# Optimization experiments

Hardware: AMD Instinct MI355X
Metric: run time of the kernel (lower is better)

## Reference

```python
import jax, jax.numpy as jnp
import numpy as np

K = 1024       # num_embeddings
D = 64         # embedding_dim
DECAY = 0.99
COMMIT = 0.25
EPS = 1e-05


def setup_inputs() -> dict:
    key = jax.random.key(0)
    k1, k2, k3 = jax.random.split(key, 3)
    x = jax.random.normal(k1, (16, 64, 64, 64), jnp.float32)  # NCHW, C == D
    embedding_weight = jax.random.normal(k2, (K, D), jnp.float32)
    ema_weight = jax.random.normal(k3, (K, D), jnp.float32)
    ema_cluster_size = jnp.zeros((K,), jnp.float32)
    return {"x": x, "embedding_weight": embedding_weight,
            "ema_cluster_size": ema_cluster_size, "ema_weight": ema_weight}


def reference(x, embedding_weight, ema_cluster_size, ema_weight):
    # NCHW -> NHWC, flatten tokens
    xp = jnp.transpose(x, (0, 2, 3, 1))            # [B,H,W,D]
    flat = xp.reshape(-1, D)                        # [N,D]
    dists = ((flat ** 2).sum(1, keepdims=True)
             + (embedding_weight ** 2).sum(1)
             - 2.0 * flat @ embedding_weight.T)     # [N,K]
    idx = jnp.argmin(dists, axis=1)                 # [N]
    encodings = jax.nn.one_hot(idx, K, dtype=flat.dtype)  # [N,K]
    quantized = jnp.take(embedding_weight, idx, axis=0).reshape(xp.shape)
    # training-mode EMA updates (scatter-add instead of dense one-hot matmuls)
    counts = jnp.zeros((K,), flat.dtype).at[idx].add(1.0)
    new_cs = ema_cluster_size * DECAY + (1.0 - DECAY) * counts
    n = new_cs.sum()
    new_cs = (new_cs + EPS) / (n + K * EPS) * n     # Laplace smoothing
    dw = jnp.zeros((K, D), flat.dtype).at[idx].add(flat)
    new_ema_weight = ema_weight * DECAY + (1.0 - DECAY) * dw
    new_embedding = new_ema_weight / new_cs[:, None]
    # commitment loss and straight-through estimator
    e_latent_loss = jnp.mean((jax.lax.stop_gradient(quantized) - xp) ** 2)
    loss = COMMIT * e_latent_loss
    q_st = xp + jax.lax.stop_gradient(quantized - xp)
    return (loss, jnp.transpose(q_st, (0, 3, 1, 2)), encodings,
            new_embedding, new_cs, new_ema_weight)
```

## Files before the change

kernel.cpp:

```cpp
#include <hip/hip_runtime.h>

#define HW 4096
#define DECAYF 0.99f
#define ONEMF 0.01f
#define EPSF 1e-5f
#define BIAS 192.0f

typedef __bf16 bf16x8 __attribute__((ext_vector_type(8)));
typedef float f32x4 __attribute__((ext_vector_type(4)));
typedef unsigned short ushort8 __attribute__((ext_vector_type(8)));

#define WS_DW     0
#define WS_COUNTS 1048576
#define WS_NCHALF 1064960
#define WS_SSE    1065984
#define WS_IDX    1066000
#define WS_EHI    1131536
#define WS_ELO    1164304

__device__ __forceinline__ float wave_reduce_add(float v) {
#pragma unroll
    for (int o = 32; o > 0; o >>= 1) v += __shfl_xor(v, o, 64);
    return v;
}

__device__ __forceinline__ unsigned short bf_rne(float f) {
    unsigned int u = __float_as_uint(f);
    unsigned int r = u + 0x7fffu + ((u >> 16) & 1u);
    return (unsigned short)(r >> 16);
}

__device__ __forceinline__ unsigned med3u(unsigned a, unsigned b, unsigned c) {
    unsigned mn = a < b ? a : b;
    unsigned mx = a > b ? a : b;
    unsigned t = mx < c ? mx : c;
    return mn > t ? mn : t;
}

__global__ __launch_bounds__(256) void prep_kernel(const float* __restrict__ E,
                                                   float* __restrict__ ws) {
    const int bid = blockIdx.x, tid = threadIdx.x;
    const int id = bid * 256 + tid;
    ws[id] = 0.0f;
    if (bid == 0 && tid == 0) ws[WS_SSE] = 0.0f;
    if (bid < 256) {
        const float v = E[id];
        const unsigned short h = bf_rne(v);
        const float hf = __uint_as_float((unsigned int)h << 16);
        const unsigned short l = bf_rne(v - hf);
        ((unsigned short*)(ws + WS_EHI))[id] = h;
        ((unsigned short*)(ws + WS_ELO))[id] = l;
        const float s = wave_reduce_add(v * v);
        if ((tid & 63) == 0) ws[WS_NCHALF + (id >> 6)] = -0.5f * s;
    }
}

__global__ __launch_bounds__(512, 4) void vq_main(const float* __restrict__ x,
                                                  const float* __restrict__ E,
                                                  float* __restrict__ out,
                                                  float* __restrict__ ws) {
    const int tid = threadIdx.x;
    const int lane = tid & 63;
    const int w = tid >> 6;
    const int wg = w & 3;
    const int kh = w >> 2;
    const int q = lane >> 4, m = lane & 15;
    const int blk = blockIdx.x;
    const int bb = blk >> 5;
    const int hw0 = (blk & 31) << 7;
    const int tok0 = blk << 7;

    __shared__ float xs[128 * 68];
    __shared__ unsigned t1s[8][32][4], t2s[8][32][4];
    __shared__ int t1c[8][32][4], t2c[8][32][4];
    __shared__ int idx_sh[128];

    {
        const float* xb = x + ((size_t)bb << 18) + hw0;
#pragma unroll
        for (int cc = 0; cc < 16; ++cc) {
            const int id = cc * 512 + tid;
            const int c = id >> 7, t = id & 127;
            xs[t * 68 + c] = xb[((size_t)c << 12) + t];
        }
    }
    __syncthreads();

    bf16x8 Ah[2][2], Al[2][2];
#pragma unroll
    for (int t = 0; t < 2; ++t) {
        const int tok = wg * 32 + t * 16 + m;
#pragma unroll
        for (int s = 0; s < 2; ++s) {
            const float* p = &xs[tok * 68 + s * 32 + q * 8];
            ushort8 hu, lu;
#pragma unroll
            for (int j = 0; j < 8; ++j) {
                const float f = p[j];
                const unsigned short h = bf_rne(f);
                const float hf = __uint_as_float((unsigned int)h << 16);
                hu[j] = h;
                lu[j] = bf_rne(f - hf);
            }
            Ah[t][s] = __builtin_bit_cast(bf16x8, hu);
            Al[t][s] = __builtin_bit_cast(bf16x8, lu);
        }
    }

    const ushort8* __restrict__ Ehp = (const ushort8*)(ws + WS_EHI);
    const ushort8* __restrict__ Elp = (const ushort8*)(ws + WS_ELO);
    const float* __restrict__ ncp = ws + WS_NCHALF;

    unsigned b1[2][4] = {{0,0,0,0},{0,0,0,0}}, b2[2][4] = {{0,0,0,0},{0,0,0,0}};

    const int ck0 = kh * 32;
    const int codeA0 = ck0 * 16 + m, codeB0 = (ck0 + 1) * 16 + m;
    ushort8 hA0 = Ehp[codeA0 * 8 + q],     hA1 = Ehp[codeA0 * 8 + 4 + q];
    ushort8 lA0 = Elp[codeA0 * 8 + q],     lA1 = Elp[codeA0 * 8 + 4 + q];
    float   ncA = ncp[codeA0];
    ushort8 hB0 = Ehp[codeB0 * 8 + q],     hB1 = Ehp[codeB0 * 8 + 4 + q];
    ushort8 lB0 = Elp[codeB0 * 8 + q],     lB1 = Elp[codeB0 * 8 + 4 + q];
    float   ncB = ncp[codeB0];

    auto compute = [&](const ushort8& h0, const ushort8& h1, const ushort8& l0,
                       const ushort8& l1, float nc, int ckv) {
        const bf16x8 bh0 = __builtin_bit_cast(bf16x8, h0);
        const bf16x8 bh1 = __builtin_bit_cast(bf16x8, h1);
        const bf16x8 bl0 = __builtin_bit_cast(bf16x8, l0);
        const bf16x8 bl1 = __builtin_bit_cast(bf16x8, l1);
        const float base = nc + BIAS;
#pragma unroll
        for (int t = 0; t < 2; ++t) {
            f32x4 acc = {base, base, base, base};
            acc = __builtin_amdgcn_mfma_f32_16x16x32_bf16(Ah[t][0], bh0, acc, 0, 0, 0);
            acc = __builtin_amdgcn_mfma_f32_16x16x32_bf16(Ah[t][1], bh1, acc, 0, 0, 0);
            acc = __builtin_amdgcn_mfma_f32_16x16x32_bf16(Al[t][0], bh0, acc, 0, 0, 0);
            acc = __builtin_amdgcn_mfma_f32_16x16x32_bf16(Al[t][1], bh1, acc, 0, 0, 0);
            acc = __builtin_amdgcn_mfma_f32_16x16x32_bf16(Ah[t][0], bl0, acc, 0, 0, 0);
            acc = __builtin_amdgcn_mfma_f32_16x16x32_bf16(Ah[t][1], bl1, acc, 0, 0, 0);
#pragma unroll
            for (int r = 0; r < 4; ++r) {
                const unsigned p = (__float_as_uint(acc[r]) & ~63u) | (unsigned)ckv;
                b2[t][r] = med3u(b1[t][r], b2[t][r], p);
                b1[t][r] = b1[t][r] > p ? b1[t][r] : p;
            }
        }
    };

    for (int j2 = 0; j2 < 16; ++j2) {
        const int ckA = ck0 + 2 * j2;
        const ushort8 ch0 = hA0, ch1 = hA1, cl0 = lA0, cl1 = lA1; const float cnc = ncA;
        {
            const int nc_ = (j2 < 15) ? (ckA + 2) * 16 + m : codeA0;
            hA0 = Ehp[nc_ * 8 + q]; hA1 = Ehp[nc_ * 8 + 4 + q];
            lA0 = Elp[nc_ * 8 + q]; lA1 = Elp[nc_ * 8 + 4 + q];
            ncA = ncp[nc_];
        }
        compute(ch0, ch1, cl0, cl1, cnc, ckA);
        const ushort8 dh0 = hB0, dh1 = hB1, dl0 = lB0, dl1 = lB1; const float dnc = ncB;
        {
            const int nc_ = (j2 < 15) ? (ckA + 3) * 16 + m : codeB0;
            hB0 = Ehp[nc_ * 8 + q]; hB1 = Ehp[nc_ * 8 + 4 + q];
            lB0 = Elp[nc_ * 8 + q]; lB1 = Elp[nc_ * 8 + 4 + q];
            ncB = ncp[nc_];
        }
        compute(dh0, dh1, dl0, dl1, dnc, ckA + 1);
    }

    int c1[2][4], c2[2][4];
#pragma unroll
    for (int t = 0; t < 2; ++t)
#pragma unroll
        for (int r = 0; r < 4; ++r) {
            c1[t][r] = (int)((b1[t][r] & 63u) << 4) | m;
            c2[t][r] = (int)((b2[t][r] & 63u) << 4) | m;
        }
#pragma unroll
    for (int d = 1; d < 4; d <<= 1) {
#pragma unroll
        for (int t = 0; t < 2; ++t)
#pragma unroll
            for (int r = 0; r < 4; ++r) {
                const unsigned o1 = __shfl_xor(b1[t][r], d, 64);
                const int      oc1 = __shfl_xor(c1[t][r], d, 64);
                const unsigned o2 = __shfl_xor(b2[t][r], d, 64);
                const int      oc2 = __shfl_xor(c2[t][r], d, 64);
                const bool win = o1 > b1[t][r];
                const unsigned n1 = win ? o1 : b1[t][r]; const int nc1 = win ? oc1 : c1[t][r];
                const unsigned ls = win ? b1[t][r] : o1; const int lc = win ? c1[t][r] : oc1;
                const unsigned os = win ? o2 : b2[t][r]; const int oc = win ? oc2 : c2[t][r];
                const bool sec = ls > os;
                b1[t][r] = n1; c1[t][r] = nc1;
                b2[t][r] = sec ? ls : os; c2[t][r] = sec ? lc : oc;
            }
    }
    if ((m & 3) == 0) {
        const int g = m >> 2;
#pragma unroll
        for (int t = 0; t < 2; ++t)
#pragma unroll
            for (int r = 0; r < 4; ++r) {
                const int trow = t * 16 + q * 4 + r;
                t1s[w][trow][g] = b1[t][r]; t1c[w][trow][g] = c1[t][r];
                t2s[w][trow][g] = b2[t][r]; t2c[w][trow][g] = c2[t][r];
            }
    }
    __syncthreads();

    float dval = 0.0f;
    if (w < 4) {
        if (lane < 32) {
            const int trow = lane;
            unsigned s1 = 0, s2 = 0;
            int cc1 = 0, cc2 = 0;
#pragma unroll
            for (int h = 0; h < 2; ++h) {
                const int ww = wg + h * 4;
#pragma unroll
                for (int g = 0; g < 4; ++g) {
                    const unsigned a = t1s[ww][trow][g]; const int ac = t1c[ww][trow][g];
                    if (a > s1) { s2 = s1; cc2 = cc1; s1 = a; cc1 = ac; }
                    else if (a > s2) { s2 = a; cc2 = ac; }
                    const unsigned bs = t2s[ww][trow][g]; const int bc = t2c[ww][trow][g];
                    if (bs > s2) { s2 = bs; cc2 = bc; }
                }
            }
            const int tokL = wg * 32 + lane;
            const int ca = cc1 < cc2 ? cc1 : cc2;
            const int cb = cc1 < cc2 ? cc2 : cc1;
            const f32x4* Ea4 = (const f32x4*)(E + ca * 64);
            const f32x4* Eb4 = (const f32x4*)(E + cb * 64);
            const f32x4* xr4 = (const f32x4*)(&xs[tokL * 68]);
            double sa = 0, ea = 0, sb = 0, eb = 0, x2 = 0;
#pragma unroll 4
            for (int c4 = 0; c4 < 16; ++c4) {
                const f32x4 ev = Ea4[c4], fv = Eb4[c4], xv4 = xr4[c4];
#pragma unroll
                for (int j = 0; j < 4; ++j) {
                    const double xv = (double)xv4[j];
                    const double va = (double)ev[j], vb = (double)fv[j];
                    sa += xv * va; ea += va * va;
                    sb += xv * vb; eb += vb * vb;
                    x2 += xv * xv;
                }
            }
            const double qa = ea - 2.0 * sa;
            const double qb = eb - 2.0 * sb;
            int best; double qq;
            if (qb < qa) { best = cb; qq = qb; } else { best = ca; qq = qa; }
            idx_sh[tokL] = best;
            ((int*)(ws + WS_IDX))[tok0 + tokL] = best;
            float dd = (float)(qq + x2);
            dval = dd < 0.f ? 0.f : dd;
            atomicAdd(&ws[WS_COUNTS + (blk & 15) * 1024 + best], 1.0f);
        }
        const float ssum = wave_reduce_add(dval);
        if (lane == 0) atomicAdd(&ws[WS_SSE], ssum);
    }
    __syncthreads();

    float* outq = out + 1;
#pragma unroll
    for (int cc = 0; cc < 16; ++cc) {
        const int id = cc * 512 + tid;
        const int c = id >> 7, t = id & 127;
        const int kb = idx_sh[t];
        const float xv = xs[t * 68 + c];
        const float eq = E[kb * 64 + c];
        outq[((size_t)(bb * 64 + c) << 12) + hw0 + t] = xv + (eq - xv);
    }
    {
        float* dwr = ws + WS_DW + (size_t)(blk & 15) * 65536;
#pragma unroll 4
        for (int tt = 0; tt < 16; ++tt) {
            const int t = w * 16 + tt;
            const int kb = idx_sh[t];
            atomicAdd(&dwr[kb * 64 + lane], xs[t * 68 + lane]);
        }
    }
}

__global__ __launch_bounds__(256) void enc_write(const float* __restrict__ ws,
                                                 float* __restrict__ out) {
    const int tid = threadIdx.x;
    const int c0 = tid << 2;
    const int row0 = blockIdx.x << 5;
    const int* __restrict__ idxp = (const int*)(ws + WS_IDX);
    float* enc = out + 1 + (size_t)4194304;
    for (int r = 0; r < 32; ++r) {
        const int row = row0 + r;
        const int kb = idxp[row];
        f32x4 v;
        v[0] = (c0 == kb) ? 1.0f : 0.0f;
        v[1] = (c0 + 1 == kb) ? 1.0f : 0.0f;
        v[2] = (c0 + 2 == kb) ? 1.0f : 0.0f;
        v[3] = (c0 + 3 == kb) ? 1.0f : 0.0f;
        *(f32x4*)(enc + (size_t)row * 1024 + c0) = v;
    }
}

__global__ __launch_bounds__(1024) void fin_cs(const float* __restrict__ cs_in,
                                               float* __restrict__ out,
                                               const float* __restrict__ ws) {
    __shared__ float red[16];
    __shared__ float n_sh;
    const int tid = threadIdx.x;
    float cnt = 0.f;
#pragma unroll
    for (int p = 0; p < 16; ++p) cnt += ws[WS_COUNTS + p * 1024 + tid];
    const float raw = cs_in[tid] * DECAYF + ONEMF * cnt;
    const float s = wave_reduce_add(raw);
    if ((tid & 63) == 0) red[tid >> 6] = s;
    __syncthreads();
    if (tid == 0) {
        float n = 0.f;
#pragma unroll
        for (int i = 0; i < 16; ++i) n += red[i];
        n_sh = n;
        out[0] = 0.25f * ws[WS_SSE] * (1.0f / 4194304.0f);
    }
    __syncthreads();
    const float n = n_sh;
    out[71368705 + tid] = (raw + EPSF) / (n + 1024.0f * EPSF) * n;
}

__global__ __launch_bounds__(256) void fin_w(const float* __restrict__ emaw,
                                             float* __restrict__ out,
                                             const float* __restrict__ ws) {
    const int i = blockIdx.x * 256 + threadIdx.x;
    float acc = 0.f;
#pragma unroll
    for (int p = 0; p < 16; ++p) acc += ws[WS_DW + p * 65536 + i];
    const float val = emaw[i] * DECAYF + ONEMF * acc;
    out[71369729 + i] = val;
    const float cs = out[71368705 + (i >> 6)];
    out[71303169 + i] = val / cs;
}

extern "C" void kernel_launch(void* const* d_in, const int* in_sizes, int n_in,
                              void* d_out, int out_size, void* d_ws, size_t ws_size,
                              hipStream_t stream) {
    const float* x    = (const float*)d_in[0];
    const float* E    = (const float*)d_in[1];
    const float* cs   = (const float*)d_in[2];
    const float* emaw = (const float*)d_in[3];
    float* out = (float*)d_out;
    float* ws  = (float*)d_ws;

    prep_kernel<<<4160, 256, 0, stream>>>(E, ws);
    vq_main<<<512, 512, 0, stream>>>(x, E, out, ws);
    enc_write<<<2048, 256, 0, stream>>>(ws, out);
    fin_cs<<<1, 1024, 0, stream>>>(cs, out, ws);
    fin_w<<<256, 256, 0, stream>>>(emaw, out, ws);
}
```

Before: 419.0 us.

## Split VQ main kernel into scoring and quantize/scatter kernels; memset workspace

Splits the fused kernel in two. vq_score now only computes the nearest-code indices and the loss. A new qst_dw kernel reloads x, gathers the codebook rows into shared memory, does the dw atomics and writes the straight-through output. Workspace zeroing moves from the prep kernel to hipMemsetAsync, and the prep grid shrinks to match. The aim is to shorten the heavy scoring kernel's tail and let the write-heavy phase run at its own occupancy, at the cost of reading x twice and one extra launch.

```diff
diff --git a/kernel.cpp b/kernel.cpp
--- a/kernel.cpp
+++ b/kernel.cpp
@@ -39,26 +39,20 @@
 
 __global__ __launch_bounds__(256) void prep_kernel(const float* __restrict__ E,
                                                    float* __restrict__ ws) {
-    const int bid = blockIdx.x, tid = threadIdx.x;
-    const int id = bid * 256 + tid;
-    ws[id] = 0.0f;
-    if (bid == 0 && tid == 0) ws[WS_SSE] = 0.0f;
-    if (bid < 256) {
-        const float v = E[id];
-        const unsigned short h = bf_rne(v);
-        const float hf = __uint_as_float((unsigned int)h << 16);
-        const unsigned short l = bf_rne(v - hf);
-        ((unsigned short*)(ws + WS_EHI))[id] = h;
-        ((unsigned short*)(ws + WS_ELO))[id] = l;
-        const float s = wave_reduce_add(v * v);
-        if ((tid & 63) == 0) ws[WS_NCHALF + (id >> 6)] = -0.5f * s;
-    }
-}
-
-__global__ __launch_bounds__(512, 4) void vq_main(const float* __restrict__ x,
-                                                  const float* __restrict__ E,
-                                                  float* __restrict__ out,
-                                                  float* __restrict__ ws) {
+    const int id = blockIdx.x * 256 + threadIdx.x;
+    const float v = E[id];
+    const unsigned short h = bf_rne(v);
+    const float hf = __uint_as_float((unsigned int)h << 16);
+    const unsigned short l = bf_rne(v - hf);
+    ((unsigned short*)(ws + WS_EHI))[id] = h;
+    ((unsigned short*)(ws + WS_ELO))[id] = l;
+    const float s = wave_reduce_add(v * v);
+    if ((threadIdx.x & 63) == 0) ws[WS_NCHALF + (id >> 6)] = -0.5f * s;
+}
+
+__global__ __launch_bounds__(512, 4) void vq_score(const float* __restrict__ x,
+                                                   const float* __restrict__ E,
+                                                   float* __restrict__ ws) {
     const int tid = threadIdx.x;
     const int lane = tid & 63;
     const int w = tid >> 6;
@@ -73,7 +67,6 @@
     __shared__ float xs[128 * 68];
     __shared__ unsigned t1s[8][32][4], t2s[8][32][4];
     __shared__ int t1c[8][32][4], t2c[8][32][4];
-    __shared__ int idx_sh[128];
 
     {
         const float* xb = x + ((size_t)bb << 18) + hw0;
@@ -248,7 +241,6 @@
             const double qb = eb - 2.0 * sb;
             int best; double qq;
             if (qb < qa) { best = cb; qq = qb; } else { best = ca; qq = qa; }
-            idx_sh[tokL] = best;
             ((int*)(ws + WS_IDX))[tok0 + tokL] = best;
             float dd = (float)(qq + x2);
             dval = dd < 0.f ? 0.f : dd;
@@ -257,26 +249,56 @@
         const float ssum = wave_reduce_add(dval);
         if (lane == 0) atomicAdd(&ws[WS_SSE], ssum);
     }
-    __syncthreads();
-
-    float* outq = out + 1;
-#pragma unroll
-    for (int cc = 0; cc < 16; ++cc) {
-        const int id = cc * 512 + tid;
-        const int c = id >> 7, t = id & 127;
-        const int kb = idx_sh[t];
-        const float xv = xs[t * 68 + c];
-        const float eq = E[kb * 64 + c];
-        outq[((size_t)(bb * 64 + c) << 12) + hw0 + t] = xv + (eq - xv);
-    }
+}
+
+__global__ __launch_bounds__(256) void qst_dw(const float* __restrict__ x,
+                                              const float* __restrict__ E,
+                                              float* __restrict__ out,
+                                              float* __restrict__ ws) {
+    const int tid = threadIdx.x;
+    const int lane = tid & 63;
+    const int w = tid >> 6;
+    const int blk = blockIdx.x;
+    const int bb = blk >> 5;
+    const int hw0 = (blk & 31) << 7;
+    const int tok0 = blk << 7;
+
+    __shared__ float xs[128 * 65];
+    __shared__ float qs[128 * 65];
+    __shared__ int idx_sh[128];
+
+    if (tid < 128) idx_sh[tid] = ((const int*)(ws + WS_IDX))[tok0 + tid];
+    {
+        const float* xb = x + ((size_t)bb << 18) + hw0;
+#pragma unroll
+        for (int cc = 0; cc < 32; ++cc) {
+            const int id = cc * 256 + tid;
+            const int c = id >> 7, t = id & 127;
+            xs[t * 65 + c] = xb[((size_t)c << 12) + t];
+        }
+    }
+    __syncthreads();
+
     {
         float* dwr = ws + WS_DW + (size_t)(blk & 15) * 65536;
 #pragma unroll 4
-        for (int tt = 0; tt < 16; ++tt) {
-            const int t = w * 16 + tt;
+        for (int tt = 0; tt < 32; ++tt) {
+            const int t = w * 32 + tt;
             const int kb = idx_sh[t];
-            atomicAdd(&dwr[kb * 64 + lane], xs[t * 68 + lane]);
-        }
+            qs[t * 65 + lane] = E[kb * 64 + lane];
+            atomicAdd(&dwr[kb * 64 + lane], xs[t * 65 + lane]);
+        }
+    }
+    __syncthreads();
+
+    float* outq = out + 1;
+#pragma unroll
+    for (int cc = 0; cc < 32; ++cc) {
+        const int id = cc * 256 + tid;
+        const int c = id >> 7, t = id & 127;
+        const float xv = xs[t * 65 + c];
+        const float eq = qs[t * 65 + c];
+        outq[((size_t)(bb * 64 + c) << 12) + hw0 + t] = xv + (eq - xv);
     }
 }
 
@@ -347,8 +369,10 @@
     float* out = (float*)d_out;
     float* ws  = (float*)d_ws;
 
-    prep_kernel<<<4160, 256, 0, stream>>>(E, ws);
-    vq_main<<<512, 512, 0, stream>>>(x, E, out, ws);
+    hipMemsetAsync(ws, 0, (size_t)(WS_SSE + 1) * sizeof(float), stream);
+    prep_kernel<<<256, 256, 0, stream>>>(E, ws);
+    vq_score<<<512, 512, 0, stream>>>(x, E, ws);
+    qst_dw<<<512, 256, 0, stream>>>(x, E, out, ws);
     enc_write<<<2048, 256, 0, stream>>>(ws, out);
     fin_cs<<<1, 1024, 0, stream>>>(cs, out, ws);
     fin_w<<<256, 256, 0, stream>>>(emaw, out, ws);
```

Measured after the change: 435.4 us. 3.9% more time.
